# Kernel optimization log

Measured on AMD Instinct MI355X. Metric: run time of the kernel, lower is better.

The kernel has to match this reference:

```python
import jax, jax.numpy as jnp
import numpy as np

IN_FEATURES = 256
OUT_FEATURES = 256
GRID_SIZE = 5
SPLINE_ORDER = 3
GRID_RANGE = (-1.0, 1.0)
LN_EPS = 1e-5


def _make_grid():
    h = (GRID_RANGE[1] - GRID_RANGE[0]) / GRID_SIZE
    n_knots = GRID_SIZE + 2 * SPLINE_ORDER + 1  # 12
    return jnp.linspace(GRID_RANGE[0] - h * SPLINE_ORDER,
                        GRID_RANGE[1] + h * SPLINE_ORDER,
                        n_knots, dtype=jnp.float32)


def setup_inputs() -> dict:
    key = jax.random.key(0)
    k1, k2, k3 = jax.random.split(key, 3)
    N = 65536
    # kaiming_uniform_(nonlinearity='linear'): bound = sqrt(3/fan_in)
    b1 = np.sqrt(3.0 / IN_FEATURES)
    fan_sp = IN_FEATURES * (GRID_SIZE + SPLINE_ORDER)
    b2 = np.sqrt(3.0 / fan_sp)
    return {
        "x": jax.random.normal(k1, (N, IN_FEATURES), dtype=jnp.float32),
        "grid": _make_grid(),
        "base_weight": jax.random.uniform(k2, (OUT_FEATURES, IN_FEATURES), jnp.float32, -b1, b1),
        "spline_weight": jax.random.uniform(k3, (OUT_FEATURES, IN_FEATURES, GRID_SIZE + SPLINE_ORDER), jnp.float32, -b2, b2),
        "ln_gamma": jnp.ones((OUT_FEATURES,), jnp.float32),
        "ln_beta": jnp.zeros((OUT_FEATURES,), jnp.float32),
        "prelu_a": jnp.full((1,), 0.25, jnp.float32),
    }


def reference(x, grid, base_weight, spline_weight, ln_gamma, ln_beta, prelu_a):
    # base branch: exact GELU then linear (matches nn.GELU() + F.linear)
    base_out = jnp.einsum('ni,oi->no', jax.nn.gelu(x, approximate=False), base_weight)

    # Cox-de Boor B-spline basis recursion. grid is identical per feature in
    # the original ([in, 12] expand of a 1D linspace) so we broadcast the 1D grid.
    xu = x[:, :, None]                                   # [N, in, 1]
    bases = ((xu >= grid[:-1]) & (xu < grid[1:])).astype(x.dtype)  # [N, in, 11]
    for k in range(1, SPLINE_ORDER + 1):
        left = grid[:-(k + 1)]
        right = grid[k:-1]
        delta = jnp.where(right == left, jnp.ones_like(right), right - left)
        bases = ((xu - left) / delta * bases[:, :, :-1]
                 + (grid[k + 1:] - xu) / (grid[k + 1:] - grid[1:-k]) * bases[:, :, 1:])
    # bases: [N, in, grid_size + spline_order]

    spline_out = jnp.einsum('nig,oig->no', bases, spline_weight)

    y = base_out + spline_out
    mu = jnp.mean(y, axis=-1, keepdims=True)
    var = jnp.mean(jnp.square(y - mu), axis=-1, keepdims=True)
    y = (y - mu) * jax.lax.rsqrt(var + LN_EPS) * ln_gamma + ln_beta
    # PReLU with a single shared slope (nn.PReLU default)
    return jnp.where(y >= 0, y, prelu_a[0] * y)
```

## Files before the change

### kernel.cpp

```cpp
#include <hip/hip_runtime.h>
#include <hip/hip_bf16.h>
#include <math.h>
#include <stdint.h>

typedef __attribute__((ext_vector_type(8))) short short8;
typedef __attribute__((ext_vector_type(8))) unsigned short u16x8;
typedef __attribute__((ext_vector_type(4))) float f32x4;

#define BM 128
#define BK 64
#define K_TOT 2304
#define NKT 36
#define A_BYTES (BM * 128)
#define W_BYTES (256 * 128)
#define LDS_TOTAL (2 * A_BYTES + 2 * W_BYTES)

__device__ __forceinline__ unsigned short f2bf(float f) {
    union { float f; unsigned u; } c; c.f = f;
    unsigned u = c.u;
    unsigned r = u + 0x7fffu + ((u >> 16) & 1u);
    return (unsigned short)(r >> 16);
}

__device__ __forceinline__ float gelu_exact(float x) {
    return 0.5f * x * (1.0f + erff(x * 0.7071067811865475f));
}

__device__ __forceinline__ int swz(int row, int u) {
    return row * 128 + ((u ^ (row & 7)) << 4);
}

__global__ void kan_prep_w(const float* __restrict__ bw, const float* __restrict__ sw,
                           unsigned short* __restrict__ Ws) {
    int U = blockIdx.x * 256 + threadIdx.x;
    if (U >= NKT * 2048) return;
    int kt = U >> 11, lu = U & 2047;
    int row = lu >> 3, s = lu & 7;
    int uu = s ^ (row & 7);
    int k = kt * 64 + uu * 8;
    u16x8 pk;
#pragma unroll
    for (int e = 0; e < 8; ++e) {
        int kk = k + e;
        float v = (kk < 256) ? bw[row * 256 + kk] : sw[row * 2048 + (kk - 256)];
        pk[e] = f2bf(v);
    }
    *(u16x8*)(Ws + (size_t)U * 8) = pk;
}

__device__ __forceinline__ void stage_tile(
    int kt, unsigned char* ldsAbuf, unsigned char* ldsWbuf,
    const float* __restrict__ X, const unsigned short* __restrict__ Wshuf,
    int row0, int t, int wid, int lane)
{
    const unsigned short* wsrc = Wshuf + ((size_t)kt * 2048 + wid * 256 + lane) * 8;
    unsigned char* wdst = ldsWbuf + wid * 4096;
#pragma unroll
    for (int r = 0; r < 4; ++r) {
        __builtin_amdgcn_global_load_lds(
            (const __attribute__((address_space(1))) void*)(wsrc + r * 512),
            (__attribute__((address_space(3))) void*)(wdst + r * 1024),
            16, 0, 0);
    }

    if (kt < 4) {
#pragma unroll
        for (int rep = 0; rep < 2; ++rep) {
            int p = t + rep * 512;
            int row = p >> 3, u = p & 7;
            const float* xp = X + (size_t)(row0 + row) * 256 + kt * 64 + u * 8;
            float4 v0 = *(const float4*)xp;
            float4 v1 = *(const float4*)(xp + 4);
            float vv[8] = {v0.x, v0.y, v0.z, v0.w, v1.x, v1.y, v1.z, v1.w};
            u16x8 pk;
#pragma unroll
            for (int j = 0; j < 8; ++j) pk[j] = f2bf(gelu_exact(vv[j]));
            *(u16x8*)(ldsAbuf + swz(row, u)) = pk;
        }
    } else {
        const int ibase = (kt - 4) * 8;
#pragma unroll
        for (int rep = 0; rep < 2; ++rep) {
            int p = t + rep * 512;
            int row = p >> 3, il = p & 7;
            float xv = X[(size_t)(row0 + row) * 256 + ibase + il];
            float xi = (xv + 2.2f) * 2.5f;
            float fi = floorf(xi);
            float tt = xi - fi;
            float s1 = 1.0f - tt;
            float t2 = tt * tt, t3 = t2 * tt;
            float w0 = s1 * s1 * s1 * (1.0f / 6.0f);
            float w1 = 0.5f * t3 - t2 + (2.0f / 3.0f);
            float w2 = -0.5f * t3 + 0.5f * t2 + 0.5f * tt + (1.0f / 6.0f);
            float w3 = t3 * (1.0f / 6.0f);
            uint64_t Wp = (uint64_t)f2bf(w0) | ((uint64_t)f2bf(w1) << 16)
                        | ((uint64_t)f2bf(w2) << 32) | ((uint64_t)f2bf(w3) << 48);
            int b = 16 * ((int)fi - 3);
            uint64_t L = (b >= 0 && b < 64) ? (Wp << b)
                       : ((b < 0 && b > -64) ? (Wp >> (-b)) : 0ull);
            uint64_t H = (b >= 64 && b < 128) ? (Wp << (b - 64))
                       : ((b > 0 && b < 64) ? (Wp >> (64 - b)) : 0ull);
            union { uint64_t q[2]; u16x8 v; } rr;
            rr.q[0] = L; rr.q[1] = H;
            *(u16x8*)(ldsAbuf + swz(row, il)) = rr.v;
        }
    }
}

__global__ __launch_bounds__(512, 2) void kan_fused(
    const float* __restrict__ X, const unsigned short* __restrict__ Wshuf,
    const float* __restrict__ gamma, const float* __restrict__ beta,
    const float* __restrict__ prelu_a, float* __restrict__ OUT)
{
    extern __shared__ __align__(16) unsigned char lds[];

    const int t = threadIdx.x;
    const int row0 = blockIdx.x * BM;
    const int wid = t >> 6, lane = t & 63;
    const int wr = wid >> 2, wc = wid & 3;
    const int lcol = lane & 15, q = lane >> 4;

    f32x4 acc[4][4];
#pragma unroll
    for (int m = 0; m < 4; ++m)
#pragma unroll
        for (int n = 0; n < 4; ++n) acc[m][n] = (f32x4){0.f, 0.f, 0.f, 0.f};

    stage_tile(0, lds, lds + 2 * A_BYTES, X, Wshuf, row0, t, wid, lane);
    __syncthreads();

    for (int kt = 0; kt < NKT; ++kt) {
        const int cur = kt & 1;
        unsigned char* A_cur = lds + cur * A_BYTES;
        unsigned char* W_cur = lds + 2 * A_BYTES + cur * W_BYTES;
        unsigned char* A_nxt = lds + (cur ^ 1) * A_BYTES;
        unsigned char* W_nxt = lds + 2 * A_BYTES + (cur ^ 1) * W_BYTES;

        short8 af[4], bfr[4];
#pragma unroll
        for (int m = 0; m < 4; ++m)
            af[m] = *(const short8*)(A_cur + swz(wr * 64 + m * 16 + lcol, q));
#pragma unroll
        for (int n = 0; n < 4; ++n)
            bfr[n] = *(const short8*)(W_cur + swz(wc * 64 + n * 16 + lcol, q));

        if (kt + 1 < NKT)
            stage_tile(kt + 1, A_nxt, W_nxt, X, Wshuf, row0, t, wid, lane);

#pragma unroll
        for (int m = 0; m < 4; ++m)
#pragma unroll
            for (int n = 0; n < 4; ++n)
                acc[m][n] = __builtin_amdgcn_mfma_f32_16x16x32_bf16(
                    af[m], bfr[n], acc[m][n], 0, 0, 0);

#pragma unroll
        for (int m = 0; m < 4; ++m)
            af[m] = *(const short8*)(A_cur + swz(wr * 64 + m * 16 + lcol, 4 + q));
#pragma unroll
        for (int n = 0; n < 4; ++n)
            bfr[n] = *(const short8*)(W_cur + swz(wc * 64 + n * 16 + lcol, 4 + q));
#pragma unroll
        for (int m = 0; m < 4; ++m)
#pragma unroll
            for (int n = 0; n < 4; ++n)
                acc[m][n] = __builtin_amdgcn_mfma_f32_16x16x32_bf16(
                    af[m], bfr[n], acc[m][n], 0, 0, 0);

        __syncthreads();
    }

    float* stats = (float*)lds;
#pragma unroll
    for (int m = 0; m < 4; ++m) {
#pragma unroll
        for (int r = 0; r < 4; ++r) {
            float s = 0.f, s2 = 0.f;
#pragma unroll
            for (int n = 0; n < 4; ++n) { float v = acc[m][n][r]; s += v; s2 += v * v; }
#pragma unroll
            for (int msk = 1; msk < 16; msk <<= 1) {
                s  += __shfl_xor(s,  msk, 64);
                s2 += __shfl_xor(s2, msk, 64);
            }
            if ((lane & 15) == (m * 4 + r)) {
                int row = wr * 64 + m * 16 + q * 4 + r;
                stats[row * 8 + wc]     = s;
                stats[row * 8 + 4 + wc] = s2;
            }
        }
    }
    __syncthreads();

    const float apr = prelu_a[0];
    float gv[4], bv[4];
#pragma unroll
    for (int n = 0; n < 4; ++n) {
        int col = wc * 64 + n * 16 + lcol;
        gv[n] = gamma[col]; bv[n] = beta[col];
    }
#pragma unroll
    for (int m = 0; m < 4; ++m) {
#pragma unroll
        for (int r = 0; r < 4; ++r) {
            int row = wr * 64 + m * 16 + q * 4 + r;
            f32x4 sv = *(const f32x4*)(stats + row * 8);
            f32x4 qv = *(const f32x4*)(stats + row * 8 + 4);
            float mu  = (sv[0] + sv[1] + sv[2] + sv[3]) * (1.0f / 256.0f);
            float ex2 = (qv[0] + qv[1] + qv[2] + qv[3]) * (1.0f / 256.0f);
            float rs = rsqrtf(ex2 - mu * mu + 1e-5f);
            float* op = OUT + (size_t)(row0 + row) * 256;
#pragma unroll
            for (int n = 0; n < 4; ++n) {
                int col = wc * 64 + n * 16 + lcol;
                float y = (acc[m][n][r] - mu) * rs * gv[n] + bv[n];
                op[col] = (y >= 0.f) ? y : apr * y;
            }
        }
    }
}

extern "C" void kernel_launch(void* const* d_in, const int* in_sizes, int n_in,
                              void* d_out, int out_size, void* d_ws, size_t ws_size,
                              hipStream_t stream) {
    const float* x  = (const float*)d_in[0];
    const float* bw = (const float*)d_in[2];
    const float* sw = (const float*)d_in[3];
    const float* g  = (const float*)d_in[4];
    const float* be = (const float*)d_in[5];
    const float* pa = (const float*)d_in[6];
    float* out = (float*)d_out;
    unsigned short* Ws = (unsigned short*)d_ws;

    hipFuncSetAttribute((const void*)kan_fused,
                        hipFuncAttributeMaxDynamicSharedMemorySize, LDS_TOTAL);

    const int Nrows = in_sizes[0] / 256;
    kan_prep_w<<<(NKT * 2048 + 255) / 256, 256, 0, stream>>>(bw, sw, Ws);
    kan_fused<<<Nrows / BM, 512, LDS_TOTAL, stream>>>(x, Ws, g, be, pa, out);
}
```

Before: 149.9 us.

## Double row tile to 256 and split X prefetch from A-tile compute

```diff
diff --git a/kernel.cpp b/kernel.cpp
--- a/kernel.cpp
+++ b/kernel.cpp
@@ -7,9 +7,8 @@
 typedef __attribute__((ext_vector_type(8))) unsigned short u16x8;
 typedef __attribute__((ext_vector_type(4))) float f32x4;
 
-#define BM 128
+#define BM 256
 #define BK 64
-#define K_TOT 2304
 #define NKT 36
 #define A_BYTES (BM * 128)
 #define W_BYTES (256 * 128)
@@ -48,11 +47,9 @@
     *(u16x8*)(Ws + (size_t)U * 8) = pk;
 }
 
-__device__ __forceinline__ void stage_tile(
-    int kt, unsigned char* ldsAbuf, unsigned char* ldsWbuf,
-    const float* __restrict__ X, const unsigned short* __restrict__ Wshuf,
-    int row0, int t, int wid, int lane)
-{
+__device__ __forceinline__ void w_issue(int kt, unsigned char* ldsWbuf,
+                                        const unsigned short* __restrict__ Wshuf,
+                                        int wid, int lane) {
     const unsigned short* wsrc = Wshuf + ((size_t)kt * 2048 + wid * 256 + lane) * 8;
     unsigned char* wdst = ldsWbuf + wid * 4096;
 #pragma unroll
@@ -62,49 +59,28 @@
             (__attribute__((address_space(3))) void*)(wdst + r * 1024),
             16, 0, 0);
     }
-
-    if (kt < 4) {
-#pragma unroll
-        for (int rep = 0; rep < 2; ++rep) {
-            int p = t + rep * 512;
-            int row = p >> 3, u = p & 7;
-            const float* xp = X + (size_t)(row0 + row) * 256 + kt * 64 + u * 8;
-            float4 v0 = *(const float4*)xp;
-            float4 v1 = *(const float4*)(xp + 4);
-            float vv[8] = {v0.x, v0.y, v0.z, v0.w, v1.x, v1.y, v1.z, v1.w};
-            u16x8 pk;
-#pragma unroll
-            for (int j = 0; j < 8; ++j) pk[j] = f2bf(gelu_exact(vv[j]));
-            *(u16x8*)(ldsAbuf + swz(row, u)) = pk;
-        }
-    } else {
-        const int ibase = (kt - 4) * 8;
-#pragma unroll
-        for (int rep = 0; rep < 2; ++rep) {
-            int p = t + rep * 512;
-            int row = p >> 3, il = p & 7;
-            float xv = X[(size_t)(row0 + row) * 256 + ibase + il];
-            float xi = (xv + 2.2f) * 2.5f;
-            float fi = floorf(xi);
-            float tt = xi - fi;
-            float s1 = 1.0f - tt;
-            float t2 = tt * tt, t3 = t2 * tt;
-            float w0 = s1 * s1 * s1 * (1.0f / 6.0f);
-            float w1 = 0.5f * t3 - t2 + (2.0f / 3.0f);
-            float w2 = -0.5f * t3 + 0.5f * t2 + 0.5f * tt + (1.0f / 6.0f);
-            float w3 = t3 * (1.0f / 6.0f);
-            uint64_t Wp = (uint64_t)f2bf(w0) | ((uint64_t)f2bf(w1) << 16)
-                        | ((uint64_t)f2bf(w2) << 32) | ((uint64_t)f2bf(w3) << 48);
-            int b = 16 * ((int)fi - 3);
-            uint64_t L = (b >= 0 && b < 64) ? (Wp << b)
-                       : ((b < 0 && b > -64) ? (Wp >> (-b)) : 0ull);
-            uint64_t H = (b >= 64 && b < 128) ? (Wp << (b - 64))
-                       : ((b > 0 && b < 64) ? (Wp >> (64 - b)) : 0ull);
-            union { uint64_t q[2]; u16x8 v; } rr;
-            rr.q[0] = L; rr.q[1] = H;
-            *(u16x8*)(ldsAbuf + swz(row, il)) = rr.v;
-        }
-    }
+}
+
+__device__ __forceinline__ u16x8 spline_row(float xv) {
+    float xi = (xv + 2.2f) * 2.5f;
+    float fi = floorf(xi);
+    float tt = xi - fi;
+    float s1 = 1.0f - tt;
+    float t2 = tt * tt, t3 = t2 * tt;
+    float w0 = s1 * s1 * s1 * (1.0f / 6.0f);
+    float w1 = 0.5f * t3 - t2 + (2.0f / 3.0f);
+    float w2 = -0.5f * t3 + 0.5f * t2 + 0.5f * tt + (1.0f / 6.0f);
+    float w3 = t3 * (1.0f / 6.0f);
+    uint64_t Wp = (uint64_t)f2bf(w0) | ((uint64_t)f2bf(w1) << 16)
+                | ((uint64_t)f2bf(w2) << 32) | ((uint64_t)f2bf(w3) << 48);
+    int b = 16 * ((int)fi - 3);
+    uint64_t L = (b >= 0 && b < 64) ? (Wp << b)
+               : ((b < 0 && b > -64) ? (Wp >> (-b)) : 0ull);
+    uint64_t H = (b >= 64 && b < 128) ? (Wp << (b - 64))
+               : ((b > 0 && b < 64) ? (Wp >> (64 - b)) : 0ull);
+    union { uint64_t q[2]; u16x8 v; } rr;
+    rr.q[0] = L; rr.q[1] = H;
+    return rr.v;
 }
 
 __global__ __launch_bounds__(512, 2) void kan_fused(
@@ -119,14 +95,33 @@
     const int wid = t >> 6, lane = t & 63;
     const int wr = wid >> 2, wc = wid & 3;
     const int lcol = lane & 15, q = lane >> 4;
-
-    f32x4 acc[4][4];
-#pragma unroll
-    for (int m = 0; m < 4; ++m)
+    const int srow = t >> 3, scol = t & 7;
+
+    f32x4 acc[8][4];
+#pragma unroll
+    for (int m = 0; m < 8; ++m)
 #pragma unroll
         for (int n = 0; n < 4; ++n) acc[m][n] = (f32x4){0.f, 0.f, 0.f, 0.f};
 
-    stage_tile(0, lds, lds + 2 * A_BYTES, X, Wshuf, row0, t, wid, lane);
+    w_issue(0, lds + 2 * A_BYTES, Wshuf, wid, lane);
+    {
+        float xg[32];
+#pragma unroll
+        for (int rep = 0; rep < 4; ++rep) {
+            const float* xp = X + (size_t)(row0 + srow + rep * 64) * 256 + scol * 8;
+            float4 v0 = *(const float4*)xp;
+            float4 v1 = *(const float4*)(xp + 4);
+            xg[rep * 8 + 0] = v0.x; xg[rep * 8 + 1] = v0.y; xg[rep * 8 + 2] = v0.z; xg[rep * 8 + 3] = v0.w;
+            xg[rep * 8 + 4] = v1.x; xg[rep * 8 + 5] = v1.y; xg[rep * 8 + 6] = v1.z; xg[rep * 8 + 7] = v1.w;
+        }
+#pragma unroll
+        for (int rep = 0; rep < 4; ++rep) {
+            u16x8 pk;
+#pragma unroll
+            for (int j = 0; j < 8; ++j) pk[j] = f2bf(gelu_exact(xg[rep * 8 + j]));
+            *(u16x8*)(lds + swz(srow + rep * 64, scol)) = pk;
+        }
+    }
     __syncthreads();
 
     for (int kt = 0; kt < NKT; ++kt) {
@@ -135,44 +130,77 @@
         unsigned char* W_cur = lds + 2 * A_BYTES + cur * W_BYTES;
         unsigned char* A_nxt = lds + (cur ^ 1) * A_BYTES;
         unsigned char* W_nxt = lds + 2 * A_BYTES + (cur ^ 1) * W_BYTES;
-
-        short8 af[4], bfr[4];
-#pragma unroll
-        for (int m = 0; m < 4; ++m)
-            af[m] = *(const short8*)(A_cur + swz(wr * 64 + m * 16 + lcol, q));
+        const bool has_next = (kt + 1 < NKT);
+        const bool nxt_gelu = (kt + 1 < 4);
+
+        float xg[32]; float xs[4];
+        if (has_next) {
+            if (nxt_gelu) {
+#pragma unroll
+                for (int rep = 0; rep < 4; ++rep) {
+                    const float* xp = X + (size_t)(row0 + srow + rep * 64) * 256
+                                    + (kt + 1) * 64 + scol * 8;
+                    float4 v0 = *(const float4*)xp;
+                    float4 v1 = *(const float4*)(xp + 4);
+                    xg[rep * 8 + 0] = v0.x; xg[rep * 8 + 1] = v0.y; xg[rep * 8 + 2] = v0.z; xg[rep * 8 + 3] = v0.w;
+                    xg[rep * 8 + 4] = v1.x; xg[rep * 8 + 5] = v1.y; xg[rep * 8 + 6] = v1.z; xg[rep * 8 + 7] = v1.w;
+                }
+            } else {
+                const int ibase = (kt + 1 - 4) * 8;
+#pragma unroll
+                for (int rep = 0; rep < 4; ++rep)
+                    xs[rep] = X[(size_t)(row0 + srow + rep * 64) * 256 + ibase + scol];
+            }
+            w_issue(kt + 1, W_nxt, Wshuf, wid, lane);
+        }
+
+        short8 af[8], bfr[4];
+#pragma unroll
+        for (int m = 0; m < 8; ++m)
+            af[m] = *(const short8*)(A_cur + swz(wr * 128 + m * 16 + lcol, q));
 #pragma unroll
         for (int n = 0; n < 4; ++n)
             bfr[n] = *(const short8*)(W_cur + swz(wc * 64 + n * 16 + lcol, q));
-
-        if (kt + 1 < NKT)
-            stage_tile(kt + 1, A_nxt, W_nxt, X, Wshuf, row0, t, wid, lane);
-
-#pragma unroll
-        for (int m = 0; m < 4; ++m)
+#pragma unroll
+        for (int m = 0; m < 8; ++m)
 #pragma unroll
             for (int n = 0; n < 4; ++n)
                 acc[m][n] = __builtin_amdgcn_mfma_f32_16x16x32_bf16(
                     af[m], bfr[n], acc[m][n], 0, 0, 0);
-
-#pragma unroll
-        for (int m = 0; m < 4; ++m)
-            af[m] = *(const short8*)(A_cur + swz(wr * 64 + m * 16 + lcol, 4 + q));
+#pragma unroll
+        for (int m = 0; m < 8; ++m)
+            af[m] = *(const short8*)(A_cur + swz(wr * 128 + m * 16 + lcol, 4 + q));
 #pragma unroll
         for (int n = 0; n < 4; ++n)
             bfr[n] = *(const short8*)(W_cur + swz(wc * 64 + n * 16 + lcol, 4 + q));
 #pragma unroll
-        for (int m = 0; m < 4; ++m)
+        for (int m = 0; m < 8; ++m)
 #pragma unroll
             for (int n = 0; n < 4; ++n)
                 acc[m][n] = __builtin_amdgcn_mfma_f32_16x16x32_bf16(
                     af[m], bfr[n], acc[m][n], 0, 0, 0);
 
+        if (has_next) {
+            if (nxt_gelu) {
+#pragma unroll
+                for (int rep = 0; rep < 4; ++rep) {
+                    u16x8 pk;
+#pragma unroll
+                    for (int j = 0; j < 8; ++j) pk[j] = f2bf(gelu_exact(xg[rep * 8 + j]));
+                    *(u16x8*)(A_nxt + swz(srow + rep * 64, scol)) = pk;
+                }
+            } else {
+#pragma unroll
+                for (int rep = 0; rep < 4; ++rep)
+                    *(u16x8*)(A_nxt + swz(srow + rep * 64, scol)) = spline_row(xs[rep]);
+            }
+        }
         __syncthreads();
     }
 
     float* stats = (float*)lds;
 #pragma unroll
-    for (int m = 0; m < 4; ++m) {
+    for (int m = 0; m < 8; ++m) {
 #pragma unroll
         for (int r = 0; r < 4; ++r) {
             float s = 0.f, s2 = 0.f;
@@ -183,8 +211,8 @@
                 s  += __shfl_xor(s,  msk, 64);
                 s2 += __shfl_xor(s2, msk, 64);
             }
-            if ((lane & 15) == (m * 4 + r)) {
-                int row = wr * 64 + m * 16 + q * 4 + r;
+            if ((lane & 15) == ((m * 4 + r) & 15)) {
+                int row = wr * 128 + m * 16 + q * 4 + r;
                 stats[row * 8 + wc]     = s;
                 stats[row * 8 + 4 + wc] = s2;
             }
@@ -200,10 +228,10 @@
         gv[n] = gamma[col]; bv[n] = beta[col];
     }
 #pragma unroll
-    for (int m = 0; m < 4; ++m) {
+    for (int m = 0; m < 8; ++m) {
 #pragma unroll
         for (int r = 0; r < 4; ++r) {
-            int row = wr * 64 + m * 16 + q * 4 + r;
+            int row = wr * 128 + m * 16 + q * 4 + r;
             f32x4 sv = *(const f32x4*)(stats + row * 8);
             f32x4 qv = *(const f32x4*)(stats + row * 8 + 4);
             float mu  = (sv[0] + sv[1] + sv[2] + sv[3]) * (1.0f / 256.0f);
```

New measurement: 136.4 us. -9.0%, faster.
